# Kernel optimization log

Measured on AMD Instinct MI355X. Metric: run time of the kernel, lower is better.

Reference implementation:

```python
import jax, jax.numpy as jnp
import numpy as np

EPS_COS = 1e-12
EPS_BN = 1e-5


def setup_inputs() -> dict:
    key = jax.random.key(0)
    k1, k2, k3 = jax.random.split(key, 3)
    B, C, H, W = 16384, 3, 32, 32
    K, NUM_CLASSES = 300, 10
    return {
        "x": jax.random.normal(k1, (B, C, H, W), dtype=jnp.float32),
        "w5": jax.random.normal(k2, (K, C, H, W), dtype=jnp.float32),
        "gamma": jnp.ones((K,), dtype=jnp.float32),
        "beta": jnp.zeros((K,), dtype=jnp.float32),
        "w6": jax.random.normal(k3, (NUM_CLASSES, K), dtype=jnp.float32),
    }


def _clp_cos_sim(x, w5):
    # kernel covers the full spatial extent -> one patch per sample.
    B = x.shape[0]
    K = w5.shape[0]
    xf = x.reshape(B, -1)                       # (B, C*H*W)
    wf = w5.reshape(K, -1)                      # (K, C*H*W)
    xn = xf / (jnp.linalg.norm(xf, axis=1, keepdims=True) + EPS_COS)
    wn = wf / (jnp.linalg.norm(wf, axis=1, keepdims=True) + EPS_COS)
    cos = jnp.einsum("bd,kd->bk", xn, wn)      # cosine similarity to each prototype
    return jax.nn.relu(cos)                     # clp: clamp negatives to 0


def reference(x, w5, gamma, beta, w6):
    # fc5: clamped cosine-similarity match against 300 prototypes -> (B, 300, 1, 1)
    fc5 = _clp_cos_sim(x, w5)[:, :, None, None]
    # bn5: BatchNorm2d(300), batch statistics (training-mode forward math)
    mean = jnp.mean(fc5, axis=(0, 2, 3), keepdims=True)
    var = jnp.var(fc5, axis=(0, 2, 3), keepdims=True)
    bn5 = gamma[None, :, None, None] * (fc5 - mean) / jnp.sqrt(var + EPS_BN) \
          + beta[None, :, None, None]
    # fc6: non-competitive 1x1 map 300 -> 10 (dot-product readout), flattened
    fc6 = jnp.einsum("bk,ok->bo", bn5[:, :, 0, 0], w6)   # (B, 10)
    return fc5, bn5, fc6
```

## Files before the change

### kernel.cpp

```cpp
#include <hip/hip_runtime.h>
#include <stdint.h>

#define BATCH 16384
#define DDIM  3072
#define NK    300
#define NKP   320
#define NCLS  10

#define BM 64
#define BN 160
#define BK 64
#define KT (DDIM / BK)

typedef __bf16 bf16x8 __attribute__((ext_vector_type(8)));
typedef float  f32x4  __attribute__((ext_vector_type(4)));

typedef __attribute__((address_space(1))) const void gvoid_as1;
typedef __attribute__((address_space(3))) void lvoid_as3;

__device__ __forceinline__ unsigned f2bf(float f) {
  unsigned u = __float_as_uint(f);
  u += 0x7FFFu + ((u >> 16) & 1u);
  return u >> 16;
}
__device__ __forceinline__ unsigned long long pack4bf(float a, float b, float c, float d) {
  unsigned lo = f2bf(a) | (f2bf(b) << 16);
  unsigned hi = f2bf(c) | (f2bf(d) << 16);
  return (unsigned long long)lo | ((unsigned long long)hi << 32);
}

__global__ __launch_bounds__(256) void prep_w_kernel(
    const float* __restrict__ w5, unsigned short* __restrict__ wn,
    float* __restrict__ rw, float* __restrict__ gsum, float* __restrict__ gsq) {
  const int r = blockIdx.x;
  const int t = threadIdx.x;
  if (r == 0) {
    for (int i = t; i < NKP; i += 256) { gsum[i] = 0.f; gsq[i] = 0.f; }
  }
  unsigned long long* dst = (unsigned long long*)(wn + (size_t)r * DDIM);
  if (r < NK) {
    const float4* src = (const float4*)(w5 + (size_t)r * DDIM);
    float ss = 0.f;
#pragma unroll
    for (int i = 0; i < 3; ++i) {
      float4 v = src[t + i * 256];
      ss += v.x * v.x + v.y * v.y + v.z * v.z + v.w * v.w;
      dst[t + i * 256] = pack4bf(v.x, v.y, v.z, v.w);
    }
#pragma unroll
    for (int m = 1; m <= 32; m <<= 1) ss += __shfl_xor(ss, m, 64);
    __shared__ float red[4];
    if ((t & 63) == 0) red[t >> 6] = ss;
    __syncthreads();
    if (t == 0) {
      float tot = red[0] + red[1] + red[2] + red[3];
      rw[r] = 1.f / (sqrtf(tot) + 1e-12f);
    }
  } else {
#pragma unroll
    for (int i = 0; i < 3; ++i) dst[t + i * 256] = 0ull;
    if (t == 0) rw[r] = 0.f;
  }
}

__global__ __launch_bounds__(512, 4) void gemm_kernel(
    const float* __restrict__ x, const unsigned short* __restrict__ wn,
    const float* __restrict__ rw, float* __restrict__ fc5,
    float* __restrict__ gsum, float* __restrict__ gsq) {
  __shared__ alignas(16) unsigned short xs[BM * BK];
  __shared__ alignas(16) unsigned short wt[BN * BK];
  __shared__ float rxs[BM];
  __shared__ float bsum[BN], bsq[BN];

  const int tid  = threadIdx.x;
  const int lane = tid & 63;
  const int w    = tid >> 6;
  const int wm   = w >> 1;
  const int wnv  = w & 1;
  const int m0   = (int)(blockIdx.x >> 1) * BM;
  const int n0   = (int)(blockIdx.x & 1) * BN;

  if (tid < BN) { bsum[tid] = 0.f; bsq[tid] = 0.f; }

  const int xr0 = tid >> 4;
  const int xc4 = tid & 15;
  const float* xrow0 = x + (size_t)(m0 + xr0) * DDIM;
  const float* xrow1 = x + (size_t)(m0 + xr0 + 32) * DDIM;
  const int xb0 = xr0 * 128 + ((((xc4 >> 1) ^ (xr0 & 7)) << 4)) + ((xc4 & 1) << 3);
  const int xb1 = (xr0 + 32) * 128 + ((((xc4 >> 1) ^ (xr0 & 7)) << 4)) + ((xc4 & 1) << 3);

  f32x4 zz = {0.f, 0.f, 0.f, 0.f};
  f32x4 acc[5];
#pragma unroll
  for (int i = 0; i < 5; ++i) acc[i] = zz;
  float ss0 = 0.f, ss1 = 0.f;

  for (int kt = 0; kt < KT; ++kt) {
    float4 v0 = *(const float4*)(xrow0 + kt * BK + xc4 * 4);
    float4 v1 = *(const float4*)(xrow1 + kt * BK + xc4 * 4);
    ss0 += v0.x * v0.x + v0.y * v0.y + v0.z * v0.z + v0.w * v0.w;
    ss1 += v1.x * v1.x + v1.y * v1.y + v1.z * v1.z + v1.w * v1.w;
    *(unsigned long long*)((char*)xs + xb0) = pack4bf(v0.x, v0.y, v0.z, v0.w);
    *(unsigned long long*)((char*)xs + xb1) = pack4bf(v1.x, v1.y, v1.z, v1.w);
    for (int i = w; i < 20; i += 8) {
      int c   = i * 64 + lane;
      int row = c >> 3;
      int clg = (c & 7) ^ (row & 7);
      const unsigned short* src = wn + (size_t)(n0 + row) * DDIM + kt * BK + clg * 8;
      __builtin_amdgcn_global_load_lds((gvoid_as1*)src,
                                       (lvoid_as3*)((char*)wt + i * 1024), 16, 0, 0);
    }
    __syncthreads();
#pragma unroll
    for (int ks = 0; ks < 2; ++ks) {
      const int ra = wm * 16 + (lane & 15);
      const int ca = (ks * 4 + (lane >> 4)) ^ (ra & 7);
      bf16x8 a = *(const bf16x8*)((const char*)xs + ra * 128 + ca * 16);
#pragma unroll
      for (int nf = 0; nf < 5; ++nf) {
        const int rb = wnv * 80 + nf * 16 + (lane & 15);
        const int cb = (ks * 4 + (lane >> 4)) ^ (rb & 7);
        bf16x8 b = *(const bf16x8*)((const char*)wt + rb * 128 + cb * 16);
        acc[nf] = __builtin_amdgcn_mfma_f32_16x16x32_bf16(a, b, acc[nf], 0, 0, 0);
      }
    }
    __syncthreads();
  }

#pragma unroll
  for (int m = 1; m <= 8; m <<= 1) {
    ss0 += __shfl_xor(ss0, m, 64);
    ss1 += __shfl_xor(ss1, m, 64);
  }
  if ((tid & 15) == 0) {
    rxs[xr0]      = 1.f / (sqrtf(ss0) + 1e-12f);
    rxs[xr0 + 32] = 1.f / (sqrtf(ss1) + 1e-12f);
  }
  __syncthreads();

  const int rgrp = lane >> 4;
  const int cl   = lane & 15;
  float rx[4];
#pragma unroll
  for (int j = 0; j < 4; ++j) rx[j] = rxs[wm * 16 + rgrp * 4 + j];
#pragma unroll
  for (int nf = 0; nf < 5; ++nf) {
    const int nl = wnv * 80 + nf * 16 + cl;
    const int ng = n0 + nl;
    const float rwv = rw[ng];
    float s = 0.f, q = 0.f;
#pragma unroll
    for (int j = 0; j < 4; ++j) {
      float v = acc[nf][j] * rx[j] * rwv;
      v = fmaxf(v, 0.f);
      if (ng < NK) fc5[(size_t)(m0 + wm * 16 + rgrp * 4 + j) * NK + ng] = v;
      s += v; q += v * v;
    }
    s += __shfl_xor(s, 16, 64); s += __shfl_xor(s, 32, 64);
    q += __shfl_xor(q, 16, 64); q += __shfl_xor(q, 32, 64);
    if (rgrp == 0) { atomicAdd(&bsum[nl], s); atomicAdd(&bsq[nl], q); }
  }
  __syncthreads();
  if (tid < BN) {
    const int ng = n0 + tid;
    if (ng < NK) { atomicAdd(&gsum[ng], bsum[tid]); atomicAdd(&gsq[ng], bsq[tid]); }
  }
}

__global__ __launch_bounds__(256) void bn_fc6_kernel(
    const float* __restrict__ fc5, const float* __restrict__ w6,
    const float* __restrict__ gamma, const float* __restrict__ beta,
    const float* __restrict__ gsum, const float* __restrict__ gsq,
    float* __restrict__ bn5, float* __restrict__ fc6) {
  __shared__ float w6s[NCLS * NK];
  __shared__ float scs[NK], shs[NK];
  const int t = threadIdx.x;
  for (int i = t; i < NCLS * NK; i += 256) w6s[i] = w6[i];
  for (int i = t; i < NK; i += 256) {
    const float invB = 1.f / (float)BATCH;
    float mean = gsum[i] * invB;
    float var  = gsq[i] * invB - mean * mean;
    var = fmaxf(var, 0.f);
    float sc = gamma[i] * rsqrtf(var + 1e-5f);
    scs[i] = sc;
    shs[i] = beta[i] - mean * sc;
  }
  __syncthreads();
  const int wv = t >> 6, l = t & 63;
  const int r = (int)blockIdx.x * 4 + wv;
  const float* frow = fc5 + (size_t)r * NK;
  float* brow = bn5 + (size_t)r * NK;
  float accv[NCLS];
#pragma unroll
  for (int o = 0; o < NCLS; ++o) accv[o] = 0.f;
#pragma unroll
  for (int i = 0; i < 5; ++i) {
    const int k = i * 64 + l;
    if (k < NK) {
      float b = frow[k] * scs[k] + shs[k];
      brow[k] = b;
#pragma unroll
      for (int o = 0; o < NCLS; ++o) accv[o] += b * w6s[o * NK + k];
    }
  }
#pragma unroll
  for (int o = 0; o < NCLS; ++o) {
    float v = accv[o];
#pragma unroll
    for (int m = 1; m <= 32; m <<= 1) v += __shfl_xor(v, m, 64);
    if (l == 0) fc6[(size_t)r * NCLS + o] = v;
  }
}

extern "C" void kernel_launch(void* const* d_in, const int* in_sizes, int n_in,
                              void* d_out, int out_size, void* d_ws, size_t ws_size,
                              hipStream_t stream) {
  const float* x     = (const float*)d_in[0];
  const float* w5    = (const float*)d_in[1];
  const float* gamma = (const float*)d_in[2];
  const float* beta  = (const float*)d_in[3];
  const float* w6    = (const float*)d_in[4];

  float* fc5 = (float*)d_out;
  float* bn5 = fc5 + (size_t)BATCH * NK;
  float* fc6 = bn5 + (size_t)BATCH * NK;

  char* ws = (char*)d_ws;
  unsigned short* wn = (unsigned short*)ws;
  float* rw   = (float*)(ws + (size_t)NKP * DDIM * 2);
  float* gsum = rw + NKP;
  float* gsq  = gsum + NKP;

  hipLaunchKernelGGL(prep_w_kernel, dim3(NKP), dim3(256), 0, stream,
                     w5, wn, rw, gsum, gsq);
  hipLaunchKernelGGL(gemm_kernel, dim3((BATCH / BM) * 2), dim3(512), 0, stream,
                     x, wn, rw, fc5, gsum, gsq);
  hipLaunchKernelGGL(bn_fc6_kernel, dim3(BATCH / 4), dim3(256), 0, stream,
                     fc5, w6, gamma, beta, gsum, gsq, bn5, fc6);
}
```

Baseline: 351.5 us.

## Cover all 320 prototypes per block with 32x32 MFMA and prefetched x

Each GEMM block now covers the full 320-wide prototype dimension, so x is read from global memory once instead of twice. The inner loop moves from 16x16x32 to 32x32x16 bf16 MFMA with 2x2 register tiles per wave across 5 waves of 320 threads. The next x tile is prefetched into registers during compute, and the trailing barrier on the last iteration is dropped. The shared-memory stats reduction is replaced by direct global atomics from each wave. The cost is higher register use and lower occupancy (launch bounds 320,2), and only 256 threads load x.

New measurement: 360.3 us. 2.5% more time.

```diff
diff --git a/kernel.cpp b/kernel.cpp
--- a/kernel.cpp
+++ b/kernel.cpp
@@ -8,12 +8,12 @@
 #define NCLS  10
 
 #define BM 64
-#define BN 160
+#define BN 320
 #define BK 64
 #define KT (DDIM / BK)
 
 typedef __bf16 bf16x8 __attribute__((ext_vector_type(8)));
-typedef float  f32x4  __attribute__((ext_vector_type(4)));
+typedef float  f32x16 __attribute__((ext_vector_type(16)));
 
 typedef __attribute__((address_space(1))) const void gvoid_as1;
 typedef __attribute__((address_space(3))) void lvoid_as3;
@@ -23,10 +23,13 @@
   u += 0x7FFFu + ((u >> 16) & 1u);
   return u >> 16;
 }
-__device__ __forceinline__ unsigned long long pack4bf(float a, float b, float c, float d) {
-  unsigned lo = f2bf(a) | (f2bf(b) << 16);
-  unsigned hi = f2bf(c) | (f2bf(d) << 16);
-  return (unsigned long long)lo | ((unsigned long long)hi << 32);
+__device__ __forceinline__ uint4 pack8bf(float4 a, float4 b) {
+  uint4 p;
+  p.x = f2bf(a.x) | (f2bf(a.y) << 16);
+  p.y = f2bf(a.z) | (f2bf(a.w) << 16);
+  p.z = f2bf(b.x) | (f2bf(b.y) << 16);
+  p.w = f2bf(b.z) | (f2bf(b.w) << 16);
+  return p;
 }
 
 __global__ __launch_bounds__(256) void prep_w_kernel(
@@ -45,7 +48,9 @@
     for (int i = 0; i < 3; ++i) {
       float4 v = src[t + i * 256];
       ss += v.x * v.x + v.y * v.y + v.z * v.z + v.w * v.w;
-      dst[t + i * 256] = pack4bf(v.x, v.y, v.z, v.w);
+      unsigned lo = f2bf(v.x) | (f2bf(v.y) << 16);
+      unsigned hi = f2bf(v.z) | (f2bf(v.w) << 16);
+      dst[t + i * 256] = (unsigned long long)lo | ((unsigned long long)hi << 32);
     }
 #pragma unroll
     for (int m = 1; m <= 32; m <<= 1) ss += __shfl_xor(ss, m, 64);
@@ -63,107 +68,117 @@
   }
 }
 
-__global__ __launch_bounds__(512, 4) void gemm_kernel(
+__global__ __launch_bounds__(320, 2) void gemm_kernel(
     const float* __restrict__ x, const unsigned short* __restrict__ wn,
     const float* __restrict__ rw, float* __restrict__ fc5,
     float* __restrict__ gsum, float* __restrict__ gsq) {
   __shared__ alignas(16) unsigned short xs[BM * BK];
   __shared__ alignas(16) unsigned short wt[BN * BK];
   __shared__ float rxs[BM];
-  __shared__ float bsum[BN], bsq[BN];
 
   const int tid  = threadIdx.x;
   const int lane = tid & 63;
   const int w    = tid >> 6;
-  const int wm   = w >> 1;
-  const int wnv  = w & 1;
-  const int m0   = (int)(blockIdx.x >> 1) * BM;
-  const int n0   = (int)(blockIdx.x & 1) * BN;
-
-  if (tid < BN) { bsum[tid] = 0.f; bsq[tid] = 0.f; }
-
-  const int xr0 = tid >> 4;
-  const int xc4 = tid & 15;
-  const float* xrow0 = x + (size_t)(m0 + xr0) * DDIM;
-  const float* xrow1 = x + (size_t)(m0 + xr0 + 32) * DDIM;
-  const int xb0 = xr0 * 128 + ((((xc4 >> 1) ^ (xr0 & 7)) << 4)) + ((xc4 & 1) << 3);
-  const int xb1 = (xr0 + 32) * 128 + ((((xc4 >> 1) ^ (xr0 & 7)) << 4)) + ((xc4 & 1) << 3);
-
-  f32x4 zz = {0.f, 0.f, 0.f, 0.f};
-  f32x4 acc[5];
-#pragma unroll
-  for (int i = 0; i < 5; ++i) acc[i] = zz;
-  float ss0 = 0.f, ss1 = 0.f;
+  const int m0   = (int)blockIdx.x * BM;
+
+  const int srow = tid >> 2;
+  const int sseg = tid & 3;
+  const float* xsrc = x + (size_t)(m0 + srow) * DDIM + sseg * 16;
+  const int wb0 = srow * 128 + ((((sseg << 1) | 0) ^ (srow & 7)) << 4);
+  const int wb1 = srow * 128 + ((((sseg << 1) | 1) ^ (srow & 7)) << 4);
+
+  const int wrow_l = lane >> 3;
+  const int wchk_l = (lane & 7) ^ wrow_l;
+  const unsigned short* wsrc_base = wn + (size_t)wrow_l * DDIM + wchk_l * 8;
+
+  const int r31   = lane & 31;
+  const int khalf = lane >> 5;
+  const int rb0 = w * 64 + r31;
+  const int rb1 = rb0 + 32;
+  const char* aA0 = (const char*)xs + (size_t)r31 * 128;
+  const char* aA1 = (const char*)xs + (size_t)(r31 + 32) * 128;
+  const char* aB0 = (const char*)wt + (size_t)rb0 * 128;
+  const char* aB1 = (const char*)wt + (size_t)rb1 * 128;
+  const int swzA = r31 & 7;
+  const int swzB0 = rb0 & 7, swzB1 = rb1 & 7;
+
+  f32x16 acc00 = {}, acc01 = {}, acc10 = {}, acc11 = {};
+  float ss = 0.f;
+
+  float4 v0, v1, v2, v3;
+  if (tid < 256) {
+    const float4* p = (const float4*)xsrc;
+    v0 = p[0]; v1 = p[1]; v2 = p[2]; v3 = p[3];
+  }
 
   for (int kt = 0; kt < KT; ++kt) {
-    float4 v0 = *(const float4*)(xrow0 + kt * BK + xc4 * 4);
-    float4 v1 = *(const float4*)(xrow1 + kt * BK + xc4 * 4);
-    ss0 += v0.x * v0.x + v0.y * v0.y + v0.z * v0.z + v0.w * v0.w;
-    ss1 += v1.x * v1.x + v1.y * v1.y + v1.z * v1.z + v1.w * v1.w;
-    *(unsigned long long*)((char*)xs + xb0) = pack4bf(v0.x, v0.y, v0.z, v0.w);
-    *(unsigned long long*)((char*)xs + xb1) = pack4bf(v1.x, v1.y, v1.z, v1.w);
-    for (int i = w; i < 20; i += 8) {
-      int c   = i * 64 + lane;
-      int row = c >> 3;
-      int clg = (c & 7) ^ (row & 7);
-      const unsigned short* src = wn + (size_t)(n0 + row) * DDIM + kt * BK + clg * 8;
+    if (tid < 256) {
+      ss += v0.x*v0.x + v0.y*v0.y + v0.z*v0.z + v0.w*v0.w
+          + v1.x*v1.x + v1.y*v1.y + v1.z*v1.z + v1.w*v1.w
+          + v2.x*v2.x + v2.y*v2.y + v2.z*v2.z + v2.w*v2.w
+          + v3.x*v3.x + v3.y*v3.y + v3.z*v3.z + v3.w*v3.w;
+      *(uint4*)((char*)xs + wb0) = pack8bf(v0, v1);
+      *(uint4*)((char*)xs + wb1) = pack8bf(v2, v3);
+    }
+#pragma unroll
+    for (int j = 0; j < 8; ++j) {
+      const int i = w * 8 + j;
+      const unsigned short* src = wsrc_base + (size_t)(8 * i) * DDIM + kt * BK;
       __builtin_amdgcn_global_load_lds((gvoid_as1*)src,
                                        (lvoid_as3*)((char*)wt + i * 1024), 16, 0, 0);
     }
     __syncthreads();
-#pragma unroll
-    for (int ks = 0; ks < 2; ++ks) {
-      const int ra = wm * 16 + (lane & 15);
-      const int ca = (ks * 4 + (lane >> 4)) ^ (ra & 7);
-      bf16x8 a = *(const bf16x8*)((const char*)xs + ra * 128 + ca * 16);
-#pragma unroll
-      for (int nf = 0; nf < 5; ++nf) {
-        const int rb = wnv * 80 + nf * 16 + (lane & 15);
-        const int cb = (ks * 4 + (lane >> 4)) ^ (rb & 7);
-        bf16x8 b = *(const bf16x8*)((const char*)wt + rb * 128 + cb * 16);
-        acc[nf] = __builtin_amdgcn_mfma_f32_16x16x32_bf16(a, b, acc[nf], 0, 0, 0);
-      }
-    }
-    __syncthreads();
-  }
-
-#pragma unroll
-  for (int m = 1; m <= 8; m <<= 1) {
-    ss0 += __shfl_xor(ss0, m, 64);
-    ss1 += __shfl_xor(ss1, m, 64);
-  }
-  if ((tid & 15) == 0) {
-    rxs[xr0]      = 1.f / (sqrtf(ss0) + 1e-12f);
-    rxs[xr0 + 32] = 1.f / (sqrtf(ss1) + 1e-12f);
-  }
+    if (kt + 1 < KT && tid < 256) {
+      const float4* p = (const float4*)(xsrc + (size_t)(kt + 1) * BK);
+      v0 = p[0]; v1 = p[1]; v2 = p[2]; v3 = p[3];
+    }
+#pragma unroll
+    for (int ks = 0; ks < 4; ++ks) {
+      const int c16 = ks * 2 + khalf;
+      bf16x8 a0 = *(const bf16x8*)(aA0 + ((c16 ^ swzA) << 4));
+      bf16x8 a1 = *(const bf16x8*)(aA1 + ((c16 ^ swzA) << 4));
+      bf16x8 b0 = *(const bf16x8*)(aB0 + ((c16 ^ swzB0) << 4));
+      bf16x8 b1 = *(const bf16x8*)(aB1 + ((c16 ^ swzB1) << 4));
+      acc00 = __builtin_amdgcn_mfma_f32_32x32x16_bf16(a0, b0, acc00, 0, 0, 0);
+      acc01 = __builtin_amdgcn_mfma_f32_32x32x16_bf16(a0, b1, acc01, 0, 0, 0);
+      acc10 = __builtin_amdgcn_mfma_f32_32x32x16_bf16(a1, b0, acc10, 0, 0, 0);
+      acc11 = __builtin_amdgcn_mfma_f32_32x32x16_bf16(a1, b1, acc11, 0, 0, 0);
+    }
+    if (kt + 1 < KT) __syncthreads();
+  }
+
+  ss += __shfl_xor(ss, 1, 64);
+  ss += __shfl_xor(ss, 2, 64);
+  if (tid < 256 && sseg == 0) rxs[srow] = 1.f / (sqrtf(ss) + 1e-12f);
   __syncthreads();
 
-  const int rgrp = lane >> 4;
-  const int cl   = lane & 15;
-  float rx[4];
-#pragma unroll
-  for (int j = 0; j < 4; ++j) rx[j] = rxs[wm * 16 + rgrp * 4 + j];
-#pragma unroll
-  for (int nf = 0; nf < 5; ++nf) {
-    const int nl = wnv * 80 + nf * 16 + cl;
-    const int ng = n0 + nl;
-    const float rwv = rw[ng];
-    float s = 0.f, q = 0.f;
-#pragma unroll
-    for (int j = 0; j < 4; ++j) {
-      float v = acc[nf][j] * rx[j] * rwv;
-      v = fmaxf(v, 0.f);
-      if (ng < NK) fc5[(size_t)(m0 + wm * 16 + rgrp * 4 + j) * NK + ng] = v;
-      s += v; q += v * v;
-    }
-    s += __shfl_xor(s, 16, 64); s += __shfl_xor(s, 32, 64);
-    q += __shfl_xor(q, 16, 64); q += __shfl_xor(q, 32, 64);
-    if (rgrp == 0) { atomicAdd(&bsum[nl], s); atomicAdd(&bsq[nl], q); }
-  }
-  __syncthreads();
-  if (tid < BN) {
-    const int ng = n0 + tid;
-    if (ng < NK) { atomicAdd(&gsum[ng], bsum[tid]); atomicAdd(&gsq[ng], bsq[tid]); }
+  const int kh4 = khalf * 4;
+  const int ng0 = w * 64 + r31;
+  const int ng1 = ng0 + 32;
+  const float rwv0 = rw[ng0];
+  const float rwv1 = rw[ng1];
+  float s0 = 0.f, q0 = 0.f, s1 = 0.f, q1 = 0.f;
+
+#define EPI(ACC, MI, NG, RWV, SV, QV)                                         \
+  _Pragma("unroll")                                                           \
+  for (int r = 0; r < 16; ++r) {                                              \
+    const int row = MI * 32 + (r & 3) + 8 * (r >> 2) + kh4;                   \
+    float v = ACC[r] * rxs[row] * RWV;                                        \
+    v = fmaxf(v, 0.f);                                                        \
+    if (NG < NK) fc5[(size_t)(m0 + row) * NK + NG] = v;                       \
+    SV += v; QV += v * v;                                                     \
+  }
+  EPI(acc00, 0, ng0, rwv0, s0, q0)
+  EPI(acc01, 0, ng1, rwv1, s1, q1)
+  EPI(acc10, 1, ng0, rwv0, s0, q0)
+  EPI(acc11, 1, ng1, rwv1, s1, q1)
+#undef EPI
+
+  s0 += __shfl_xor(s0, 32, 64); q0 += __shfl_xor(q0, 32, 64);
+  s1 += __shfl_xor(s1, 32, 64); q1 += __shfl_xor(q1, 32, 64);
+  if (lane < 32) {
+    atomicAdd(&gsum[ng0], s0); atomicAdd(&gsq[ng0], q0);
+    if (ng1 < NK) { atomicAdd(&gsum[ng1], s1); atomicAdd(&gsq[ng1], q1); }
   }
 }
 
@@ -233,7 +248,7 @@
 
   hipLaunchKernelGGL(prep_w_kernel, dim3(NKP), dim3(256), 0, stream,
                      w5, wn, rw, gsum, gsq);
-  hipLaunchKernelGGL(gemm_kernel, dim3((BATCH / BM) * 2), dim3(512), 0, stream,
+  hipLaunchKernelGGL(gemm_kernel, dim3(BATCH / BM), dim3(320), 0, stream,
                      x, wn, rw, fc5, gsum, gsq);
   hipLaunchKernelGGL(bn_fc6_kernel, dim3(BATCH / 4), dim3(256), 0, stream,
                      fc5, w6, gamma, beta, gsum, gsq, bn5, fc6);
```
